# Performance work log

Hardware: AMD Instinct MI355X
Metric: run time of the kernel (lower is better)

Reference implementation:

```python
import jax, jax.numpy as jnp
import numpy as np

N, E = 50000, 800000
F_IN, HID, HEADS, OUT = 128, 32, 4, 16
NEG_SLOPE = 0.2  # PyG GATConv default leaky_relu slope


def segment_softmax(logits, seg, n):
    # numerically stable softmax over edges grouped by destination node
    m = jax.ops.segment_max(logits, seg, num_segments=n)          # [N,H]
    m = jnp.where(jnp.isfinite(m), m, 0.0)                        # guard empty segments
    e = jnp.exp(logits - m[seg])                                  # [E,H]
    s = jax.ops.segment_sum(e, seg, num_segments=n)               # [N,H]
    return e / (s[seg] + 1e-16)


def gat_conv(x, W, a_src, a_dst, bias, src, dst, concat):
    H, C = a_src.shape
    n = x.shape[0]
    h = (x @ W).reshape(n, H, C)                                  # [N,H,C]
    alpha_src = jnp.einsum('nhc,hc->nh', h, a_src)                # [N,H]
    alpha_dst = jnp.einsum('nhc,hc->nh', h, a_dst)                # [N,H]
    e = jax.nn.leaky_relu(alpha_src[src] + alpha_dst[dst], NEG_SLOPE)  # [E,H]
    alpha = segment_softmax(e, dst, n)                            # [E,H]
    msg = h[src] * alpha[:, :, None]                              # [E,H,C]
    out = jax.ops.segment_sum(msg, dst, num_segments=n)           # [N,H,C]
    out = out.reshape(n, H * C) if concat else out.mean(axis=1)
    return out + bias


def setup_inputs() -> dict:
    key = jax.random.key(0)
    ks = jax.random.split(key, 12)
    s = 0.1  # keep attention logits in a sane range
    return {
        'x': jax.random.normal(ks[0], (N, F_IN), jnp.float32),
        'edge_index': jax.random.randint(ks[1], (2, E), 0, N),
        'Wemb': jax.random.normal(ks[2], (F_IN, HID), jnp.float32) * s,
        'bemb': jnp.zeros((HID,), jnp.float32),
        'W1': jax.random.normal(ks[3], (HID, HEADS * HID), jnp.float32) * s,
        'a_src1': jax.random.normal(ks[4], (HEADS, HID), jnp.float32) * s,
        'a_dst1': jax.random.normal(ks[5], (HEADS, HID), jnp.float32) * s,
        'b1': jnp.zeros((HEADS * HID,), jnp.float32),
        'W2': jax.random.normal(ks[6], (HEADS * HID, HEADS * OUT), jnp.float32) * s,
        'a_src2': jax.random.normal(ks[7], (HEADS, OUT), jnp.float32) * s,
        'a_dst2': jax.random.normal(ks[8], (HEADS, OUT), jnp.float32) * s,
        'b2': jnp.zeros((OUT,), jnp.float32),
    }


def reference(x, edge_index, Wemb, bemb, W1, a_src1, a_dst1, b1, W2, a_src2, a_dst2, b2):
    src, dst = edge_index[0], edge_index[1]
    h = x @ Wemb + bemb  # dropout layers are identity at inference
    h = jax.nn.elu(gat_conv(h, W1, a_src1, a_dst1, b1, src, dst, True))
    h = gat_conv(h, W2, a_src2, a_dst2, b2, src, dst, False)
    return jax.nn.log_softmax(h, axis=1)
```

## Files before the change

### kernel.cpp

```cpp
#include <hip/hip_runtime.h>

#define N_NODES 50000
#define N_EDGES 800000
#define F_IN    128
#define HID     32
#define HEADS   4
#define OUT_C   16

#define NBKT 196
#define CAP  5120
#define EPB  4096
#define NB64 782

typedef __attribute__((ext_vector_type(8))) short bf16x8;
typedef __attribute__((ext_vector_type(4))) float f32x4;

__device__ __forceinline__ unsigned short f2bf(float f) {
    unsigned int u = __float_as_uint(f);
    u += 0x7FFFu + ((u >> 16) & 1u);
    return (unsigned short)(u >> 16);
}
__device__ __forceinline__ float bf_lo(unsigned int u) { return __uint_as_float(u << 16); }
__device__ __forceinline__ float bf_hi(unsigned int u) { return __uint_as_float(u & 0xFFFF0000u); }
__device__ __forceinline__ float bf2f(unsigned short s) {
    return __uint_as_float(((unsigned int)s) << 16);
}

__device__ __forceinline__ float edge_w(float asv, float adv) {
    float v = asv + adv;
    v = (v > 0.f) ? v : 0.2f * v;
    return __expf(v);
}

__global__ __launch_bounds__(256) void k_F1(const float* __restrict__ x,
                                            const float* __restrict__ Wemb,
                                            const float* __restrict__ bemb,
                                            const float* __restrict__ W1,
                                            const float* __restrict__ a_src,
                                            const float* __restrict__ a_dst,
                                            unsigned short* __restrict__ h0b,
                                            float* __restrict__ as, float* __restrict__ ad,
                                            const int* __restrict__ ei,
                                            int* __restrict__ gcnt,
                                            unsigned int* __restrict__ pairs) {
    __shared__ float xs[64][132];
    __shared__ float Wl[F_IN][HID];
    __shared__ float bl[HID];
    __shared__ float vs[HID][4];
    __shared__ float vd[HID][4];
    __shared__ int hist[NBKT];
    __shared__ int base[NBKT];
    int t = threadIdx.x;
    if (blockIdx.x < NB64) {
        int node0 = blockIdx.x * 64;
        if (t < HID) bl[t] = bemb[t];
        {
            int k = (t & 127) >> 2, h = t & 3;
            const float* wrow = W1 + k * 128 + h * 32;
            const float* arow = ((t < 128) ? a_src : a_dst) + h * 32;
            float accv = 0.f;
            #pragma unroll
            for (int c2 = 0; c2 < 32; c2++) accv += wrow[c2] * arow[c2];
            if (t < 128) vs[k][h] = accv; else vd[k][h] = accv;
        }
        #pragma unroll
        for (int it = 0; it < 4; it++) {
            int idx = it * 256 + t;
            *(float4*)((float*)Wl + idx * 4) = *(const float4*)(Wemb + idx * 4);
        }
        #pragma unroll
        for (int it = 0; it < 8; it++) {
            int idx = it * 256 + t;
            int row = idx >> 5, c4 = idx & 31;
            float4 v = make_float4(0.f, 0.f, 0.f, 0.f);
            if (node0 + row < N_NODES) v = *(const float4*)(x + (size_t)(node0 + row) * F_IN + c4 * 4);
            *(float4*)&xs[row][c4 * 4] = v;
        }
        __syncthreads();
        int c = t & 7, g = t >> 3;
        float acc[2][4] = {};
        for (int k = 0; k < F_IN; k++) {
            float4 w4 = *(const float4*)&Wl[k][c * 4];
            #pragma unroll
            for (int n = 0; n < 2; n++) {
                float xv = xs[g * 2 + n][k];
                acc[n][0] += xv * w4.x; acc[n][1] += xv * w4.y;
                acc[n][2] += xv * w4.z; acc[n][3] += xv * w4.w;
            }
        }
        float ps[2][4], pd[2][4];
        #pragma unroll
        for (int n = 0; n < 2; n++) {
            float o0 = acc[n][0] + bl[c * 4];
            float o1 = acc[n][1] + bl[c * 4 + 1];
            float o2 = acc[n][2] + bl[c * 4 + 2];
            float o3 = acc[n][3] + bl[c * 4 + 3];
            int node = node0 + g * 2 + n;
            if (node < N_NODES) {
                ushort4 ob;
                ob.x = f2bf(o0); ob.y = f2bf(o1); ob.z = f2bf(o2); ob.w = f2bf(o3);
                *(ushort4*)(h0b + (size_t)node * HID + c * 4) = ob;
            }
            #pragma unroll
            for (int h = 0; h < 4; h++) {
                ps[n][h] = o0 * vs[c * 4][h] + o1 * vs[c * 4 + 1][h]
                         + o2 * vs[c * 4 + 2][h] + o3 * vs[c * 4 + 3][h];
                pd[n][h] = o0 * vd[c * 4][h] + o1 * vd[c * 4 + 1][h]
                         + o2 * vd[c * 4 + 2][h] + o3 * vd[c * 4 + 3][h];
            }
        }
        #pragma unroll
        for (int mask = 1; mask <= 4; mask <<= 1) {
            #pragma unroll
            for (int n = 0; n < 2; n++) {
                #pragma unroll
                for (int h = 0; h < 4; h++) {
                    ps[n][h] += __shfl_xor(ps[n][h], mask, 64);
                    pd[n][h] += __shfl_xor(pd[n][h], mask, 64);
                }
            }
        }
        if (c == 0) {
            #pragma unroll
            for (int n = 0; n < 2; n++) {
                int node = node0 + g * 2 + n;
                if (node < N_NODES) {
                    *(float4*)(as + node * 4) = make_float4(ps[n][0], ps[n][1], ps[n][2], ps[n][3]);
                    *(float4*)(ad + node * 4) = make_float4(pd[n][0], pd[n][1], pd[n][2], pd[n][3]);
                }
            }
        }
    } else {
        int e0 = (blockIdx.x - NB64) * EPB;
        for (int i = t; i < NBKT; i += 256) hist[i] = 0;
        __syncthreads();
        unsigned int p[16];
        int bb[16];
        #pragma unroll
        for (int i = 0; i < 16; i++) {
            int e = e0 + i * 256 + t;
            bb[i] = -1;
            if (e < N_EDGES) {
                int s = ei[e], d = ei[N_EDGES + e];
                p[i] = ((unsigned int)s << 8) | (unsigned int)(d & 255);
                bb[i] = d >> 8;
                atomicAdd(&hist[bb[i]], 1);
            }
        }
        __syncthreads();
        for (int i = t; i < NBKT; i += 256) {
            int c = hist[i];
            base[i] = i * CAP + (c ? atomicAdd(&gcnt[i], c) : 0);
            hist[i] = 0;
        }
        __syncthreads();
        #pragma unroll
        for (int i = 0; i < 16; i++) {
            if (bb[i] >= 0) {
                int off = atomicAdd(&hist[bb[i]], 1);
                pairs[base[bb[i]] + off] = p[i];
            }
        }
    }
}

__global__ __launch_bounds__(256) void k_F2(const unsigned int* __restrict__ pairs,
                                            const int* __restrict__ gcnt,
                                            int* __restrict__ rowptr,
                                            int* __restrict__ esrc) {
    __shared__ int cnt[256];
    __shared__ int cur[256];
    __shared__ int wsum[4];
    int t = threadIdx.x;
    int b = blockIdx.x;
    int lane = t & 63, wv = t >> 6;
    int v0 = (t < NBKT && t < b) ? gcnt[t] : 0;
    #pragma unroll
    for (int mask = 1; mask < 64; mask <<= 1) v0 += __shfl_xor(v0, mask, 64);
    if (lane == 0) wsum[wv] = v0;
    __syncthreads();
    int base = wsum[0] + wsum[1] + wsum[2] + wsum[3];
    int n0 = b << 8;
    int cntb = gcnt[b];
    int s0 = b * CAP;
    cnt[t] = 0;
    __syncthreads();
    for (int i = t; i < cntb; i += 256) atomicAdd(&cnt[pairs[s0 + i] & 255], 1);
    __syncthreads();
    int v = cnt[t], x = v;
    #pragma unroll
    for (int off = 1; off < 64; off <<= 1) { int y = __shfl_up(x, off, 64); if (lane >= off) x += y; }
    __syncthreads();
    if (lane == 63) wsum[wv] = x;
    __syncthreads();
    int add = 0;
    for (int j = 0; j < wv; j++) add += wsum[j];
    int excl = base + (x - v) + add;
    cur[t] = excl;
    if (n0 + t < N_NODES) rowptr[n0 + t] = excl;
    if (b == 0 && t == 0) rowptr[N_NODES] = N_EDGES;
    __syncthreads();
    for (int i = t; i < cntb; i += 256) {
        unsigned int p = pairs[s0 + i];
        int pos = atomicAdd(&cur[p & 255], 1);
        esrc[pos] = (int)(p >> 8);
    }
}

__global__ __launch_bounds__(256) void k_gather1(const int* __restrict__ esrc,
                                                 const int* __restrict__ rowptr,
                                                 const unsigned int* __restrict__ h0b,
                                                 const float* __restrict__ as,
                                                 const float* __restrict__ ad,
                                                 unsigned int* __restrict__ awb) {
    int t = threadIdx.x;
    int node = blockIdx.x * 4 + (t >> 6);
    int lane = t & 63;
    int head = lane >> 4;
    int cp = lane & 15;
    int s16 = lane >> 2;
    int h4 = lane & 3;
    int lb = cp * 4;
    int hb = head * 4;
    int beg = rowptr[node], end = rowptr[node + 1];
    float ad_w = ad[node * 4 + h4];
    float ax = 0.f, ay = 0.f, s = 0.f;
    const char* hc = (const char*)h0b;
    for (int k = beg; k < end; k += 16) {
        int idx = k + s16;
        int sm = esrc[min(idx, end - 1)];
#define G1L(J) int sj##J = __builtin_amdgcn_readlane(sm, (J) * 4); \
        unsigned int u##J = *(const unsigned int*)(hc + (size_t)(unsigned)sj##J * 64 + lb);
        G1L(0)  G1L(1)  G1L(2)  G1L(3)  G1L(4)  G1L(5)  G1L(6)  G1L(7)
        G1L(8)  G1L(9)  G1L(10) G1L(11) G1L(12) G1L(13) G1L(14) G1L(15)
#undef G1L
        float wm = edge_w(as[sm * 4 + h4], ad_w);
        if (idx >= end) wm = 0.f;
        int wmi = __float_as_int(wm);
#define G1W(J) float w##J = __int_as_float(__builtin_amdgcn_ds_bpermute(hb + (J) * 16, wmi));
        G1W(0)  G1W(1)  G1W(2)  G1W(3)  G1W(4)  G1W(5)  G1W(6)  G1W(7)
        G1W(8)  G1W(9)  G1W(10) G1W(11) G1W(12) G1W(13) G1W(14) G1W(15)
#undef G1W
        ax += bf_lo(u0)  * w0  + bf_lo(u1)  * w1  + bf_lo(u2)  * w2  + bf_lo(u3)  * w3
            + bf_lo(u4)  * w4  + bf_lo(u5)  * w5  + bf_lo(u6)  * w6  + bf_lo(u7)  * w7
            + bf_lo(u8)  * w8  + bf_lo(u9)  * w9  + bf_lo(u10) * w10 + bf_lo(u11) * w11
            + bf_lo(u12) * w12 + bf_lo(u13) * w13 + bf_lo(u14) * w14 + bf_lo(u15) * w15;
        ay += bf_hi(u0)  * w0  + bf_hi(u1)  * w1  + bf_hi(u2)  * w2  + bf_hi(u3)  * w3
            + bf_hi(u4)  * w4  + bf_hi(u5)  * w5  + bf_hi(u6)  * w6  + bf_hi(u7)  * w7
            + bf_hi(u8)  * w8  + bf_hi(u9)  * w9  + bf_hi(u10) * w10 + bf_hi(u11) * w11
            + bf_hi(u12) * w12 + bf_hi(u13) * w13 + bf_hi(u14) * w14 + bf_hi(u15) * w15;
        s += (w0 + w1 + w2 + w3) + (w4 + w5 + w6 + w7)
           + (w8 + w9 + w10 + w11) + (w12 + w13 + w14 + w15);
    }
    float rs = 1.0f / (s + 1e-16f);
    awb[(size_t)node * 64 + lane] = ((unsigned int)f2bf(ay * rs) << 16) | (unsigned int)f2bf(ax * rs);
}

__global__ __launch_bounds__(256) void k_h12(const unsigned int* __restrict__ awb,
                                             const float* __restrict__ W1,
                                             const float* __restrict__ b1,
                                             const float* __restrict__ W2,
                                             const float* __restrict__ a_src,
                                             const float* __restrict__ a_dst,
                                             unsigned short* __restrict__ h2,
                                             float* __restrict__ as, float* __restrict__ ad) {
    __shared__ unsigned int xsu[64][68];
    __shared__ unsigned short w1t[128][40];
    __shared__ unsigned short w2t[64][136];
    __shared__ float b1s[128];
    int t = threadIdx.x;
    int node0 = blockIdx.x * 64;
    if (t < 128) b1s[t] = b1[t];
    #pragma unroll
    for (int it = 0; it < 4; it++) {
        int idx = it * 256 + t;
        int row = idx >> 4, c4 = idx & 15;
        uint4 v = make_uint4(0u, 0u, 0u, 0u);
        if (node0 + row < N_NODES) v = *(const uint4*)(awb + (size_t)(node0 + row) * 64 + c4 * 4);
        *(uint4*)&xsu[row][c4 * 4] = v;
    }
    #pragma unroll
    for (int it = 0; it < 16; it++) {
        int idx = it * 256 + t;
        int k = idx >> 7, n = idx & 127;
        w1t[n][k] = f2bf(W1[idx]);
    }
    #pragma unroll
    for (int it = 0; it < 8; it++) {
        int idx = it * 256 + t;
        int k = idx >> 4, n4 = idx & 15;
        float4 w = *(const float4*)(W2 + k * 64 + n4 * 4);
        w2t[n4 * 4 + 0][k] = f2bf(w.x);
        w2t[n4 * 4 + 1][k] = f2bf(w.y);
        w2t[n4 * 4 + 2][k] = f2bf(w.z);
        w2t[n4 * 4 + 3][k] = f2bf(w.w);
    }
    __syncthreads();
    int lane = t & 63, wv = t >> 6;
    int lrow = lane & 15, lk = lane >> 4;
    const char* abase = (const char*)&xsu[wv * 16 + lrow][0];
    f32x4 o1[8];
    #pragma unroll
    for (int nt = 0; nt < 8; nt++) {
        int kt = nt >> 1;
        bf16x8 af = *(const bf16x8*)(abase + kt * 64 + lk * 16);
        bf16x8 bf1 = *(const bf16x8*)((const char*)&w1t[nt * 16 + lrow][0] + lk * 16);
        f32x4 z = {};
        o1[nt] = __builtin_amdgcn_mfma_f32_16x16x32_bf16(af, bf1, z, 0, 0, 0);
    }
    __syncthreads();
    unsigned short* o1t = (unsigned short*)&xsu[0][0];
    #pragma unroll
    for (int nt = 0; nt < 8; nt++) {
        float bb = b1s[nt * 16 + lrow];
        #pragma unroll
        for (int r = 0; r < 4; r++) {
            int noderow = wv * 16 + lk * 4 + r;
            float v = o1[nt][r] + bb;
            v = (v > 0.f) ? v : (__expf(v) - 1.0f);
            o1t[noderow * 136 + nt * 16 + lrow] = f2bf(v);
        }
    }
    __syncthreads();
    f32x4 acc[4] = {};
    const char* xbase = (const char*)&o1t[(wv * 16 + lrow) * 136];
    #pragma unroll
    for (int kt = 0; kt < 4; kt++) {
        bf16x8 af = *(const bf16x8*)(xbase + kt * 64 + lk * 16);
        #pragma unroll
        for (int h = 0; h < 4; h++) {
            bf16x8 bfr = *(const bf16x8*)((const char*)&w2t[h * 16 + lrow][0] + kt * 64 + lk * 16);
            acc[h] = __builtin_amdgcn_mfma_f32_16x16x32_bf16(af, bfr, acc[h], 0, 0, 0);
        }
    }
    float av[4], dv[4];
    #pragma unroll
    for (int h = 0; h < 4; h++) { av[h] = a_src[h * 16 + lrow]; dv[h] = a_dst[h * 16 + lrow]; }
    #pragma unroll
    for (int r = 0; r < 4; r++) {
        int node = node0 + wv * 16 + lk * 4 + r;
        float psh[4], pdh[4];
        #pragma unroll
        for (int h = 0; h < 4; h++) {
            float v = acc[h][r];
            if (node < N_NODES) h2[(size_t)node * 64 + h * 16 + lrow] = f2bf(v);
            float p = v * av[h], q = v * dv[h];
            #pragma unroll
            for (int mask = 1; mask < 16; mask <<= 1) {
                p += __shfl_xor(p, mask, 64);
                q += __shfl_xor(q, mask, 64);
            }
            psh[h] = p; pdh[h] = q;
        }
        if (lrow == 0 && node < N_NODES) {
            *(float4*)(as + node * 4) = make_float4(psh[0], psh[1], psh[2], psh[3]);
            *(float4*)(ad + node * 4) = make_float4(pdh[0], pdh[1], pdh[2], pdh[3]);
        }
    }
}

__global__ __launch_bounds__(256) void k_gather2(const int* __restrict__ esrc,
                                                 const int* __restrict__ rowptr,
                                                 const unsigned short* __restrict__ h2,
                                                 const float* __restrict__ as,
                                                 const float* __restrict__ ad,
                                                 const float* __restrict__ b2,
                                                 float* __restrict__ out) {
    int t = threadIdx.x;
    int node = blockIdx.x * 4 + (t >> 6);
    int lane = t & 63;
    int head = lane >> 4, c = lane & 15;
    int s16 = lane >> 2;
    int h4 = lane & 3;
    int lb = lane * 2;
    int hb = head * 4;
    int beg = rowptr[node], end = rowptr[node + 1];
    float ad_w = ad[node * 4 + h4];
    float acc = 0.f, s = 0.f;
    const char* h2c = (const char*)h2;
    for (int k = beg; k < end; k += 16) {
        int idx = k + s16;
        int sm = esrc[min(idx, end - 1)];
#define G2L(J) int sj##J = __builtin_amdgcn_readlane(sm, (J) * 4); \
        float r##J = bf2f(*(const unsigned short*)(h2c + (size_t)(unsigned)sj##J * 128 + lb));
        G2L(0)  G2L(1)  G2L(2)  G2L(3)  G2L(4)  G2L(5)  G2L(6)  G2L(7)
        G2L(8)  G2L(9)  G2L(10) G2L(11) G2L(12) G2L(13) G2L(14) G2L(15)
#undef G2L
        float wm = edge_w(as[sm * 4 + h4], ad_w);
        if (idx >= end) wm = 0.f;
        int wmi = __float_as_int(wm);
#define G2W(J) float w##J = __int_as_float(__builtin_amdgcn_ds_bpermute(hb + (J) * 16, wmi));
        G2W(0)  G2W(1)  G2W(2)  G2W(3)  G2W(4)  G2W(5)  G2W(6)  G2W(7)
        G2W(8)  G2W(9)  G2W(10) G2W(11) G2W(12) G2W(13) G2W(14) G2W(15)
#undef G2W
        acc += r0 * w0 + r1 * w1 + r2 * w2 + r3 * w3
             + r4 * w4 + r5 * w5 + r6 * w6 + r7 * w7
             + r8 * w8 + r9 * w9 + r10 * w10 + r11 * w11
             + r12 * w12 + r13 * w13 + r14 * w14 + r15 * w15;
        s += (w0 + w1 + w2 + w3) + (w4 + w5 + w6 + w7)
           + (w8 + w9 + w10 + w11) + (w12 + w13 + w14 + w15);
    }
    float v = acc * (1.0f / (s + 1e-16f));
    v += __shfl_xor(v, 16, 64);
    v += __shfl_xor(v, 32, 64);
    v = v * 0.25f + b2[c];
    float m = v;
    #pragma unroll
    for (int mask = 1; mask < 16; mask <<= 1) m = fmaxf(m, __shfl_xor(m, mask, 64));
    float ex = __expf(v - m);
    float se = ex;
    #pragma unroll
    for (int mask = 1; mask < 16; mask <<= 1) se += __shfl_xor(se, mask, 64);
    float res = (v - m) - __logf(se);
    if (lane < 16) out[(size_t)node * 16 + lane] = res;
}

extern "C" void kernel_launch(void* const* d_in, const int* in_sizes, int n_in,
                              void* d_out, int out_size, void* d_ws, size_t ws_size,
                              hipStream_t stream) {
    const float* x      = (const float*)d_in[0];
    const int*   ei     = (const int*)d_in[1];
    const float* Wemb   = (const float*)d_in[2];
    const float* bemb   = (const float*)d_in[3];
    const float* W1     = (const float*)d_in[4];
    const float* a_src1 = (const float*)d_in[5];
    const float* a_dst1 = (const float*)d_in[6];
    const float* b1     = (const float*)d_in[7];
    const float* W2     = (const float*)d_in[8];
    const float* a_src2 = (const float*)d_in[9];
    const float* a_dst2 = (const float*)d_in[10];
    const float* b2     = (const float*)d_in[11];
    float* out = (float*)d_out;

    char* ws = (char*)d_ws;
    size_t off = 0;
    auto alloc = [&](size_t bytes) { char* p = ws + off; off += (bytes + 255) & ~size_t(255); return p; };
    unsigned short* h2b   = (unsigned short*)alloc((size_t)N_NODES * 64 * 2);
    unsigned int*   awb   = (unsigned int*)alloc((size_t)N_NODES * 64 * 4);
    unsigned short* h0b = (unsigned short*)alloc((size_t)N_NODES * HID * 2);
    int*          esrc  = (int*)alloc((size_t)N_EDGES * 4 + 64);
    unsigned int* pairs = (unsigned int*)alloc((size_t)NBKT * CAP * 4);
    float* as     = (float*)alloc((size_t)N_NODES * 4 * 4);
    float* ad     = (float*)alloc((size_t)N_NODES * 4 * 4);
    int*   rowptr = (int*)alloc((size_t)(N_NODES + 1) * 4);
    int*   gcnt   = (int*)alloc((size_t)NBKT * 4);

    const int GB = N_NODES / 4;

    hipMemsetAsync(gcnt, 0, (size_t)NBKT * 4, stream);
    k_F1<<<NB64 + NBKT, 256, 0, stream>>>(x, Wemb, bemb, W1, a_src1, a_dst1,
                                          h0b, as, ad, ei, gcnt, pairs);
    k_F2<<<NBKT, 256, 0, stream>>>(pairs, gcnt, rowptr, esrc);
    k_gather1<<<GB, 256, 0, stream>>>(esrc, rowptr, (const unsigned int*)h0b, as, ad, awb);
    k_h12<<<NB64, 256, 0, stream>>>(awb, W1, b1, W2, a_src2, a_dst2, h2b, as, ad);
    k_gather2<<<GB, 256, 0, stream>>>(esrc, rowptr, h2b, as, ad, b2, out);
}
```

Measured before the change: 192.8 us.

## Remap gather lanes so each quarter-wave loads whole rows of four edges

Both gather kernels now split the wave into four quarters, each handling a different edge per step. Every lane loads a wider slice of a row, so there are 4 gathered loads per 16 edges instead of 16 narrow ones. Per-quarter partial sums are combined with cross-lane shuffles at the end, and in layer 2 the outputs are redistributed back to channel lanes. This cuts the number of scattered memory instructions. The cost is more ds_bpermute traffic and extra reduction and shuffle code after the loop.

```diff
diff --git a/kernel.cpp b/kernel.cpp
--- a/kernel.cpp
+++ b/kernel.cpp
@@ -216,44 +216,67 @@
     int t = threadIdx.x;
     int node = blockIdx.x * 4 + (t >> 6);
     int lane = t & 63;
-    int head = lane >> 4;
+    int q = lane >> 4;
     int cp = lane & 15;
     int s16 = lane >> 2;
     int h4 = lane & 3;
-    int lb = cp * 4;
-    int hb = head * 4;
+    int cpb = cp * 4;
+    int qb = q * 16;
     int beg = rowptr[node], end = rowptr[node + 1];
     float ad_w = ad[node * 4 + h4];
-    float ax = 0.f, ay = 0.f, s = 0.f;
+    float ax0 = 0.f, ax1 = 0.f, ax2 = 0.f, ax3 = 0.f;
+    float ay0 = 0.f, ay1 = 0.f, ay2 = 0.f, ay3 = 0.f;
+    float sacc = 0.f;
     const char* hc = (const char*)h0b;
     for (int k = beg; k < end; k += 16) {
         int idx = k + s16;
         int sm = esrc[min(idx, end - 1)];
-#define G1L(J) int sj##J = __builtin_amdgcn_readlane(sm, (J) * 4); \
-        unsigned int u##J = *(const unsigned int*)(hc + (size_t)(unsigned)sj##J * 64 + lb);
-        G1L(0)  G1L(1)  G1L(2)  G1L(3)  G1L(4)  G1L(5)  G1L(6)  G1L(7)
-        G1L(8)  G1L(9)  G1L(10) G1L(11) G1L(12) G1L(13) G1L(14) G1L(15)
-#undef G1L
         float wm = edge_w(as[sm * 4 + h4], ad_w);
         if (idx >= end) wm = 0.f;
+        sacc += wm;
         int wmi = __float_as_int(wm);
-#define G1W(J) float w##J = __int_as_float(__builtin_amdgcn_ds_bpermute(hb + (J) * 16, wmi));
-        G1W(0)  G1W(1)  G1W(2)  G1W(3)  G1W(4)  G1W(5)  G1W(6)  G1W(7)
-        G1W(8)  G1W(9)  G1W(10) G1W(11) G1W(12) G1W(13) G1W(14) G1W(15)
-#undef G1W
-        ax += bf_lo(u0)  * w0  + bf_lo(u1)  * w1  + bf_lo(u2)  * w2  + bf_lo(u3)  * w3
-            + bf_lo(u4)  * w4  + bf_lo(u5)  * w5  + bf_lo(u6)  * w6  + bf_lo(u7)  * w7
-            + bf_lo(u8)  * w8  + bf_lo(u9)  * w9  + bf_lo(u10) * w10 + bf_lo(u11) * w11
-            + bf_lo(u12) * w12 + bf_lo(u13) * w13 + bf_lo(u14) * w14 + bf_lo(u15) * w15;
-        ay += bf_hi(u0)  * w0  + bf_hi(u1)  * w1  + bf_hi(u2)  * w2  + bf_hi(u3)  * w3
-            + bf_hi(u4)  * w4  + bf_hi(u5)  * w5  + bf_hi(u6)  * w6  + bf_hi(u7)  * w7
-            + bf_hi(u8)  * w8  + bf_hi(u9)  * w9  + bf_hi(u10) * w10 + bf_hi(u11) * w11
-            + bf_hi(u12) * w12 + bf_hi(u13) * w13 + bf_hi(u14) * w14 + bf_hi(u15) * w15;
-        s += (w0 + w1 + w2 + w3) + (w4 + w5 + w6 + w7)
-           + (w8 + w9 + w10 + w11) + (w12 + w13 + w14 + w15);
-    }
-    float rs = 1.0f / (s + 1e-16f);
-    awb[(size_t)node * 64 + lane] = ((unsigned int)f2bf(ay * rs) << 16) | (unsigned int)f2bf(ax * rs);
+        int r0 = __builtin_amdgcn_ds_bpermute(qb,       sm);
+        int r1 = __builtin_amdgcn_ds_bpermute(qb + 64,  sm);
+        int r2 = __builtin_amdgcn_ds_bpermute(qb + 128, sm);
+        int r3 = __builtin_amdgcn_ds_bpermute(qb + 192, sm);
+        unsigned int u0 = *(const unsigned int*)(hc + (size_t)(unsigned)r0 * 64 + cpb);
+        unsigned int u1 = *(const unsigned int*)(hc + (size_t)(unsigned)r1 * 64 + cpb);
+        unsigned int u2 = *(const unsigned int*)(hc + (size_t)(unsigned)r2 * 64 + cpb);
+        unsigned int u3 = *(const unsigned int*)(hc + (size_t)(unsigned)r3 * 64 + cpb);
+#define BW(J,H) __int_as_float(__builtin_amdgcn_ds_bpermute(qb + (J)*64 + (H)*4, wmi))
+        float w00 = BW(0,0), w01 = BW(0,1), w02 = BW(0,2), w03 = BW(0,3);
+        float w10 = BW(1,0), w11 = BW(1,1), w12 = BW(1,2), w13 = BW(1,3);
+        float w20 = BW(2,0), w21 = BW(2,1), w22 = BW(2,2), w23 = BW(2,3);
+        float w30 = BW(3,0), w31 = BW(3,1), w32 = BW(3,2), w33 = BW(3,3);
+#undef BW
+        float la0 = bf_lo(u0), hb0 = bf_hi(u0);
+        float la1 = bf_lo(u1), hb1 = bf_hi(u1);
+        float la2 = bf_lo(u2), hb2 = bf_hi(u2);
+        float la3 = bf_lo(u3), hb3 = bf_hi(u3);
+        ax0 += la0 * w00 + la1 * w10 + la2 * w20 + la3 * w30;
+        ay0 += hb0 * w00 + hb1 * w10 + hb2 * w20 + hb3 * w30;
+        ax1 += la0 * w01 + la1 * w11 + la2 * w21 + la3 * w31;
+        ay1 += hb0 * w01 + hb1 * w11 + hb2 * w21 + hb3 * w31;
+        ax2 += la0 * w02 + la1 * w12 + la2 * w22 + la3 * w32;
+        ay2 += hb0 * w02 + hb1 * w12 + hb2 * w22 + hb3 * w32;
+        ax3 += la0 * w03 + la1 * w13 + la2 * w23 + la3 * w33;
+        ay3 += hb0 * w03 + hb1 * w13 + hb2 * w23 + hb3 * w33;
+    }
+    #pragma unroll
+    for (int m = 4; m <= 32; m <<= 1) sacc += __shfl_xor(sacc, m, 64);
+    ax0 += __shfl_xor(ax0, 16, 64); ax0 += __shfl_xor(ax0, 32, 64);
+    ax1 += __shfl_xor(ax1, 16, 64); ax1 += __shfl_xor(ax1, 32, 64);
+    ax2 += __shfl_xor(ax2, 16, 64); ax2 += __shfl_xor(ax2, 32, 64);
+    ax3 += __shfl_xor(ax3, 16, 64); ax3 += __shfl_xor(ax3, 32, 64);
+    ay0 += __shfl_xor(ay0, 16, 64); ay0 += __shfl_xor(ay0, 32, 64);
+    ay1 += __shfl_xor(ay1, 16, 64); ay1 += __shfl_xor(ay1, 32, 64);
+    ay2 += __shfl_xor(ay2, 16, 64); ay2 += __shfl_xor(ay2, 32, 64);
+    ay3 += __shfl_xor(ay3, 16, 64); ay3 += __shfl_xor(ay3, 32, 64);
+    float axf = (q == 0) ? ax0 : (q == 1) ? ax1 : (q == 2) ? ax2 : ax3;
+    float ayf = (q == 0) ? ay0 : (q == 1) ? ay1 : (q == 2) ? ay2 : ay3;
+    float sT = __int_as_float(__builtin_amdgcn_ds_bpermute(q * 4, __float_as_int(sacc)));
+    float rs = 1.0f / (sT + 1e-16f);
+    awb[(size_t)node * 64 + lane] = ((unsigned int)f2bf(ayf * rs) << 16) | (unsigned int)f2bf(axf * rs);
 }
 
 __global__ __launch_bounds__(256) void k_h12(const unsigned int* __restrict__ awb,
@@ -344,13 +367,13 @@
         for (int h = 0; h < 4; h++) {
             float v = acc[h][r];
             if (node < N_NODES) h2[(size_t)node * 64 + h * 16 + lrow] = f2bf(v);
-            float p = v * av[h], q = v * dv[h];
+            float p = v * av[h], qv = v * dv[h];
             #pragma unroll
             for (int mask = 1; mask < 16; mask <<= 1) {
                 p += __shfl_xor(p, mask, 64);
-                q += __shfl_xor(q, mask, 64);
-            }
-            psh[h] = p; pdh[h] = q;
+                qv += __shfl_xor(qv, mask, 64);
+            }
+            psh[h] = p; pdh[h] = qv;
         }
         if (lrow == 0 && node < N_NODES) {
             *(float4*)(as + node * 4) = make_float4(psh[0], psh[1], psh[2], psh[3]);
@@ -369,41 +392,60 @@
     int t = threadIdx.x;
     int node = blockIdx.x * 4 + (t >> 6);
     int lane = t & 63;
-    int head = lane >> 4, c = lane & 15;
+    int q = lane >> 4;
+    int cp = lane & 15;
+    int hcd = cp >> 2;
     int s16 = lane >> 2;
     int h4 = lane & 3;
-    int lb = lane * 2;
-    int hb = head * 4;
+    int qb = q * 16;
+    int wb = qb + hcd * 4;
     int beg = rowptr[node], end = rowptr[node + 1];
     float ad_w = ad[node * 4 + h4];
-    float acc = 0.f, s = 0.f;
-    const char* h2c = (const char*)h2;
+    float a0 = 0.f, a1 = 0.f, a2 = 0.f, a3 = 0.f, sacc = 0.f;
+    const char* pc = (const char*)h2;
     for (int k = beg; k < end; k += 16) {
         int idx = k + s16;
         int sm = esrc[min(idx, end - 1)];
-#define G2L(J) int sj##J = __builtin_amdgcn_readlane(sm, (J) * 4); \
-        float r##J = bf2f(*(const unsigned short*)(h2c + (size_t)(unsigned)sj##J * 128 + lb));
-        G2L(0)  G2L(1)  G2L(2)  G2L(3)  G2L(4)  G2L(5)  G2L(6)  G2L(7)
-        G2L(8)  G2L(9)  G2L(10) G2L(11) G2L(12) G2L(13) G2L(14) G2L(15)
-#undef G2L
         float wm = edge_w(as[sm * 4 + h4], ad_w);
         if (idx >= end) wm = 0.f;
+        sacc += wm;
         int wmi = __float_as_int(wm);
-#define G2W(J) float w##J = __int_as_float(__builtin_amdgcn_ds_bpermute(hb + (J) * 16, wmi));
-        G2W(0)  G2W(1)  G2W(2)  G2W(3)  G2W(4)  G2W(5)  G2W(6)  G2W(7)
-        G2W(8)  G2W(9)  G2W(10) G2W(11) G2W(12) G2W(13) G2W(14) G2W(15)
-#undef G2W
-        acc += r0 * w0 + r1 * w1 + r2 * w2 + r3 * w3
-             + r4 * w4 + r5 * w5 + r6 * w6 + r7 * w7
-             + r8 * w8 + r9 * w9 + r10 * w10 + r11 * w11
-             + r12 * w12 + r13 * w13 + r14 * w14 + r15 * w15;
-        s += (w0 + w1 + w2 + w3) + (w4 + w5 + w6 + w7)
-           + (w8 + w9 + w10 + w11) + (w12 + w13 + w14 + w15);
-    }
-    float v = acc * (1.0f / (s + 1e-16f));
+        int r0 = __builtin_amdgcn_ds_bpermute(qb,       sm);
+        int r1 = __builtin_amdgcn_ds_bpermute(qb + 64,  sm);
+        int r2 = __builtin_amdgcn_ds_bpermute(qb + 128, sm);
+        int r3 = __builtin_amdgcn_ds_bpermute(qb + 192, sm);
+        uint2 u0 = *(const uint2*)(pc + (size_t)(unsigned)r0 * 128 + cp * 8);
+        uint2 u1 = *(const uint2*)(pc + (size_t)(unsigned)r1 * 128 + cp * 8);
+        uint2 u2 = *(const uint2*)(pc + (size_t)(unsigned)r2 * 128 + cp * 8);
+        uint2 u3 = *(const uint2*)(pc + (size_t)(unsigned)r3 * 128 + cp * 8);
+        float w0 = __int_as_float(__builtin_amdgcn_ds_bpermute(wb,       wmi));
+        float w1 = __int_as_float(__builtin_amdgcn_ds_bpermute(wb + 64,  wmi));
+        float w2 = __int_as_float(__builtin_amdgcn_ds_bpermute(wb + 128, wmi));
+        float w3 = __int_as_float(__builtin_amdgcn_ds_bpermute(wb + 192, wmi));
+        a0 += bf_lo(u0.x) * w0 + bf_lo(u1.x) * w1 + bf_lo(u2.x) * w2 + bf_lo(u3.x) * w3;
+        a1 += bf_hi(u0.x) * w0 + bf_hi(u1.x) * w1 + bf_hi(u2.x) * w2 + bf_hi(u3.x) * w3;
+        a2 += bf_lo(u0.y) * w0 + bf_lo(u1.y) * w1 + bf_lo(u2.y) * w2 + bf_lo(u3.y) * w3;
+        a3 += bf_hi(u0.y) * w0 + bf_hi(u1.y) * w1 + bf_hi(u2.y) * w2 + bf_hi(u3.y) * w3;
+    }
+    #pragma unroll
+    for (int m = 4; m <= 32; m <<= 1) sacc += __shfl_xor(sacc, m, 64);
+    a0 += __shfl_xor(a0, 16, 64); a0 += __shfl_xor(a0, 32, 64);
+    a1 += __shfl_xor(a1, 16, 64); a1 += __shfl_xor(a1, 32, 64);
+    a2 += __shfl_xor(a2, 16, 64); a2 += __shfl_xor(a2, 32, 64);
+    a3 += __shfl_xor(a3, 16, 64); a3 += __shfl_xor(a3, 32, 64);
+    float sT = __int_as_float(__builtin_amdgcn_ds_bpermute(hcd * 4, sacc == sacc ? __float_as_int(sacc) : 0));
+    float rs = 1.0f / (sT + 1e-16f);
+    a0 *= rs; a1 *= rs; a2 *= rs; a3 *= rs;
+    int ra = (lane >> 2) * 4;
+    float t0 = __int_as_float(__builtin_amdgcn_ds_bpermute(ra, __float_as_int(a0)));
+    float t1 = __int_as_float(__builtin_amdgcn_ds_bpermute(ra, __float_as_int(a1)));
+    float t2 = __int_as_float(__builtin_amdgcn_ds_bpermute(ra, __float_as_int(a2)));
+    float t3 = __int_as_float(__builtin_amdgcn_ds_bpermute(ra, __float_as_int(a3)));
+    int e = lane & 3;
+    float v = (e == 0) ? t0 : (e == 1) ? t1 : (e == 2) ? t2 : t3;
     v += __shfl_xor(v, 16, 64);
     v += __shfl_xor(v, 32, 64);
-    v = v * 0.25f + b2[c];
+    v = v * 0.25f + b2[lane & 15];
     float m = v;
     #pragma unroll
     for (int mask = 1; mask < 16; mask <<= 1) m = fmaxf(m, __shfl_xor(m, mask, 64));
```

After: 205.1 us. +6.4%, slower.
